# Kernel tuning notes

Hardware: AMD Instinct MI355X
Metric: run time of the kernel (lower is better)

Reference implementation:

```python
import jax, jax.numpy as jnp
import numpy as np

# FreqDecoupledBlock: Mamba(d_model=dim, d_state=16, d_conv=4, expand=2) spatial branch
# + rFFT2 magnitude filter (1x1 conv -> ReLU -> 1x1 conv) branch, fused, then two 1x1 heads.

D_STATE = 16
D_CONV = 4
EXPAND = 2


def setup_inputs() -> dict:
    key = jax.random.key(0)
    B, C, H, W = 4, 64, 128, 128
    d_model = C
    d_inner = EXPAND * d_model
    dt_rank = (d_model + 15) // 16
    ks = jax.random.split(key, 18)
    g = lambda k, shp, sc: jax.random.normal(k, shp, jnp.float32) * sc
    return {
        "x": g(ks[0], (B, C, H, W), 1.0),
        # Mamba params (in_proj/x_proj/out_proj are bias-free as in mamba_ssm defaults)
        "W_in": g(ks[1], (d_model, 2 * d_inner), d_model ** -0.5),
        "conv_w": g(ks[2], (d_inner, D_CONV), 0.3),
        "conv_b": g(ks[3], (d_inner,), 0.1),
        "W_xproj": g(ks[4], (d_inner, dt_rank + 2 * D_STATE), d_inner ** -0.5),
        "W_dt": g(ks[5], (dt_rank, d_inner), dt_rank ** -0.5),
        "b_dt": g(ks[6], (d_inner,), 0.3) - 4.0,  # softplus -> small positive dt
        "A_log": jnp.tile(jnp.log(jnp.arange(1.0, D_STATE + 1.0, dtype=jnp.float32)), (d_inner, 1)),
        "D": jnp.ones((d_inner,), jnp.float32),
        "W_out": g(ks[7], (d_inner, d_model), d_inner ** -0.5),
        # freq_filter: Conv2d(C,C,1) -> ReLU -> Conv2d(C,C,1)
        "Wf1": g(ks[8], (C, C), C ** -0.5), "bf1": g(ks[9], (C,), 0.05),
        "Wf2": g(ks[10], (C, C), C ** -0.5), "bf2": g(ks[11], (C,), 0.05),
        # output heads
        "W_enh": g(ks[12], (C, C), C ** -0.5), "b_enh": g(ks[13], (C,), 0.05),
        "W_seg": g(ks[14], (C, C), C ** -0.5), "b_seg": g(ks[15], (C,), 0.05),
    }


def _silu(v):
    return v * jax.nn.sigmoid(v)


def _mamba(xf, W_in, conv_w, conv_b, W_xproj, W_dt, b_dt, A_log, D, W_out):
    # xf: (B, L, d_model)
    B, L, _ = xf.shape
    d_inner = W_in.shape[1] // 2
    dt_rank = W_dt.shape[0]
    d_state = A_log.shape[1]
    xz = xf @ W_in                                   # (B,L,2*d_inner)
    x_in, z = jnp.split(xz, 2, axis=-1)
    # depthwise causal conv1d (kernel D_CONV) along L
    xp = jnp.pad(x_in, ((0, 0), (D_CONV - 1, 0), (0, 0)))
    xc = conv_b
    for k in range(D_CONV):
        xc = xc + conv_w[:, k] * xp[:, k:k + L, :]
    xc = _silu(xc)                                   # (B,L,d_inner)
    dbc = xc @ W_xproj
    dt = jax.nn.softplus(dbc[..., :dt_rank] @ W_dt + b_dt)      # (B,L,d_inner)
    Bm = dbc[..., dt_rank:dt_rank + d_state]                    # (B,L,d_state)
    Cm = dbc[..., dt_rank + d_state:]                           # (B,L,d_state)
    A = -jnp.exp(A_log)                                          # (d_inner,d_state)

    def step(h, inps):
        xt, dtt, Bt, Ct = inps                       # (B,d_inner),(B,d_inner),(B,d_state),(B,d_state)
        dA = jnp.exp(dtt[..., None] * A)             # (B,d_inner,d_state)
        h = h * dA + (dtt * xt)[..., None] * Bt[:, None, :]
        y = jnp.einsum('bds,bs->bd', h, Ct)
        return h, y

    h0 = jnp.zeros((B, d_inner, d_state), xf.dtype)
    seq = (xc.transpose(1, 0, 2), dt.transpose(1, 0, 2), Bm.transpose(1, 0, 2), Cm.transpose(1, 0, 2))
    _, ys = jax.lax.scan(step, h0, seq)              # (L,B,d_inner)
    y = ys.transpose(1, 0, 2) + xc * D
    y = y * _silu(z)
    return y @ W_out                                 # (B,L,d_model)


def _conv1x1(v, Wc, bc):
    return jnp.einsum('oc,bchw->bohw', Wc, v) + bc[:, None, None]


def reference(x, W_in, conv_w, conv_b, W_xproj, W_dt, b_dt, A_log, D, W_out,
              Wf1, bf1, Wf2, bf2, W_enh, b_enh, W_seg, b_seg):
    B, C, H, W = x.shape
    # spatial branch: Mamba over flattened H*W tokens
    xf = x.transpose(0, 2, 3, 1).reshape(B, H * W, C)
    x_spatial = _mamba(xf, W_in, conv_w, conv_b, W_xproj, W_dt, b_dt, A_log, D, W_out)
    x_spatial = x_spatial.reshape(B, H, W, C).transpose(0, 3, 1, 2)
    # frequency branch: filter magnitude, keep phase
    Xf = jnp.fft.rfft2(x)                            # (B,C,H,W//2+1) complex
    mag = jnp.abs(Xf)
    pha = jnp.angle(Xf)
    m = jax.nn.relu(_conv1x1(mag, Wf1, bf1))
    m = _conv1x1(m, Wf2, bf2)
    x_freq = jnp.fft.irfft2(m * jnp.exp(1j * pha), s=(H, W))
    fused = x_spatial + x_freq
    feat_enh = _conv1x1(fused, W_enh, b_enh)
    feat_seg = _conv1x1(fused, W_seg, b_seg)
    return (feat_enh, feat_seg)
```

## Files before the change

kernel.cpp:

```cpp
#include <hip/hip_runtime.h>
#include <math.h>

#define BATCH 4
#define CMOD 64
#define HH 128
#define WW 128
#define LSEQ 16384
#define DI 128
#define DSTATE 16
#define DTR 4
#define TCH 64
#define NCHUNK 256

__device__ __forceinline__ float siluf(float v){ return v / (1.f + expf(-v)); }

__global__ void k_prep_w(const float* __restrict__ W_in, const float* __restrict__ W_out,
                         const float* __restrict__ W_xproj,
                         float* __restrict__ WT_in, float* __restrict__ WoT, float* __restrict__ WxT){
  int tid = blockIdx.x*256 + threadIdx.x;
  int stride = gridDim.x*256;
  for (int i=tid; i<256*64; i+=stride){ int o=i>>6, c=i&63; WT_in[i] = W_in[c*256+o]; }
  for (int i=tid; i<64*128; i+=stride){ int o=i>>7, c=i&127; WoT[i] = W_out[c*64+o]; }
  for (int i=tid; i<36*128; i+=stride){ int n=i>>7, c=i&127; WxT[i] = W_xproj[c*36+n]; }
}

__global__ __launch_bounds__(256) void k_in_proj(const float* __restrict__ x,
                                                 const float* __restrict__ WT,
                                                 float* __restrict__ xz){
  __shared__ float sm[256*33];
  int tid  = threadIdx.x;
  int bid  = blockIdx.x;
  int s8   = bid >> 6;
  int xcd  = bid & 7;
  int j    = (bid >> 3) & 7;
  int tile = s8*8 + xcd;
  int q    = j;
  size_t px = (size_t)tile*256 + tid;
  int b = (int)(px >> 14);
  int l = (int)(px & 16383);
  const float* xb = x + (((size_t)b*64)<<14) + l;
  float in[64];
  #pragma unroll
  for (int c=0;c<64;c++) in[c] = xb[((size_t)c)<<14];
  const float* Wq = WT + q*32*64;
  for (int og=0; og<8; ++og){
    const float* w0 = Wq + (og*4+0)*64;
    const float* w1 = Wq + (og*4+1)*64;
    const float* w2 = Wq + (og*4+2)*64;
    const float* w3 = Wq + (og*4+3)*64;
    float a0=0.f,a1=0.f,a2=0.f,a3=0.f;
    #pragma unroll
    for (int c=0;c<64;++c){
      float v = in[c];
      a0 = fmaf(v, w0[c], a0); a1 = fmaf(v, w1[c], a1);
      a2 = fmaf(v, w2[c], a2); a3 = fmaf(v, w3[c], a3);
    }
    float* s = sm + tid*33 + og*4;
    s[0]=a0; s[1]=a1; s[2]=a2; s[3]=a3;
  }
  __syncthreads();
  size_t rowbase = (size_t)tile*256*256 + (size_t)q*32;
  #pragma unroll
  for (int i=0;i<8;i++){
    int idx = i*256 + tid;
    int r   = idx >> 3;
    int c4  = idx & 7;
    const float* s = sm + r*33 + c4*4;
    ((float4*)(xz + rowbase + (size_t)r*256))[c4] = make_float4(s[0],s[1],s[2],s[3]);
  }
}

__global__ void k_conv_silu(const float* __restrict__ xz, const float* __restrict__ conv_w,
                            const float* __restrict__ conv_b, float* __restrict__ xc){
  size_t gid = (size_t)blockIdx.x*256 + threadIdx.x;
  int d = (int)(gid & 127);
  int l = (int)((gid >> 7) & (LSEQ-1));
  int b = (int)(gid >> 21);
  const float* base = xz + (((size_t)b)<<14)*256;
  float acc = conv_b[d];
  #pragma unroll
  for (int k=0;k<4;k++){
    int li = l + k - 3;
    if (li >= 0) acc = fmaf(conv_w[d*4+k], base[(size_t)li*256 + d], acc);
  }
  xc[gid] = siluf(acc);
}

__global__ __launch_bounds__(256) void k_xproj_dt(const float* __restrict__ xc,
                         const float* __restrict__ WxT, const float* __restrict__ W_dt,
                         const float* __restrict__ b_dt,
                         float* __restrict__ dtb, float* __restrict__ Bm, float* __restrict__ Cm){
  int tile = blockIdx.x & 255;
  int q    = blockIdx.x >> 8;
  int tid  = threadIdx.x;
  size_t px = (size_t)tile*256 + tid;
  const float4* row = (const float4*)(xc + px*128);
  if (q < 2){
    __shared__ float sout[256*17];
    #pragma unroll
    for (int half=0; half<2; ++half){
      float acc[8];
      #pragma unroll
      for (int n=0;n<8;n++) acc[n]=0.f;
      const float* Wbase = WxT + (4 + q*16 + half*8)*128;
      #pragma unroll 4
      for (int c4=0; c4<32; c4++){
        float4 v = row[c4];
        #pragma unroll
        for (int n=0;n<8;n++){
          const float4 w = *(const float4*)(Wbase + n*128 + c4*4);
          acc[n] = fmaf(v.w, w.w, fmaf(v.z, w.z, fmaf(v.y, w.y, fmaf(v.x, w.x, acc[n]))));
        }
      }
      float* s = sout + tid*17 + half*8;
      #pragma unroll
      for (int n=0;n<8;n++) s[n] = acc[n];
    }
    __syncthreads();
    float* dst = (q==0 ? Bm : Cm) + (size_t)tile*256*16;
    #pragma unroll
    for (int i=0;i<16;i++){
      int idx = i*256 + tid;
      int r = idx >> 4, j = idx & 15;
      dst[r*16 + j] = sout[r*17 + j];
    }
  } else {
    float d0=0.f,d1=0.f,d2=0.f,d3=0.f;
    #pragma unroll 4
    for (int c4=0; c4<32; c4++){
      float4 v = row[c4];
      const float4 w0 = *(const float4*)(WxT + 0*128 + c4*4);
      const float4 w1 = *(const float4*)(WxT + 1*128 + c4*4);
      const float4 w2 = *(const float4*)(WxT + 2*128 + c4*4);
      const float4 w3 = *(const float4*)(WxT + 3*128 + c4*4);
      d0 = fmaf(v.w, w0.w, fmaf(v.z, w0.z, fmaf(v.y, w0.y, fmaf(v.x, w0.x, d0))));
      d1 = fmaf(v.w, w1.w, fmaf(v.z, w1.z, fmaf(v.y, w1.y, fmaf(v.x, w1.x, d1))));
      d2 = fmaf(v.w, w2.w, fmaf(v.z, w2.z, fmaf(v.y, w2.y, fmaf(v.x, w2.x, d2))));
      d3 = fmaf(v.w, w3.w, fmaf(v.z, w3.z, fmaf(v.y, w3.y, fmaf(v.x, w3.x, d3))));
    }
    float4* dtout = (float4*)(dtb + px*128);
    for (int dg=0; dg<32; dg++){
      float r[4];
      #pragma unroll
      for (int j=0;j<4;j++){
        int d = dg*4+j;
        float v = b_dt[d];
        v = fmaf(d0, W_dt[0*128+d], v);
        v = fmaf(d1, W_dt[1*128+d], v);
        v = fmaf(d2, W_dt[2*128+d], v);
        v = fmaf(d3, W_dt[3*128+d], v);
        r[j] = (v > 20.f) ? v : log1pf(expf(v));
      }
      dtout[dg] = make_float4(r[0],r[1],r[2],r[3]);
    }
  }
}

__global__ __launch_bounds__(128) void k_scan1(const float* __restrict__ dtb, const float* __restrict__ xc,
                      const float* __restrict__ Bm, const float* __restrict__ A_log,
                      float* __restrict__ S, float* __restrict__ E1){
  int d = threadIdx.x;
  int ck = blockIdx.x & (NCHUNK-1);
  int b  = blockIdx.x >> 8;
  int t0 = ck*TCH;
  float a0 = -expf(A_log[d*16]);
  __shared__ float sB[16][16];
  float h[16];
  #pragma unroll
  for (int s=0;s<16;s++) h[s]=0.f;
  float dtsum = 0.f;
  size_t rowbase = ((size_t)b<<14);
  for (int tt=0; tt<TCH; tt+=16){
    __syncthreads();
    for (int i=threadIdx.x; i<256; i+=128){
      int tr=i>>4, s=i&15;
      sB[tr][s] = Bm[(rowbase + t0+tt+tr)*16 + s];
    }
    __syncthreads();
    for (int q=0;q<16;q++){
      size_t t = rowbase + t0+tt+q;
      float dtv = dtb[t*128 + d];
      float xcv = xc [t*128 + d];
      float e1 = expf(dtv * a0);
      float du = dtv * xcv;
      dtsum += dtv;
      float f = e1;
      #pragma unroll
      for (int s=0;s<16;s++){ h[s] = fmaf(h[s], f, du*sB[q][s]); f *= e1; }
    }
  }
  size_t idx = (((size_t)b*DI + d)<<8) + ck;
  E1[idx] = expf(dtsum*a0);
  float4* Sp = (float4*)(S + idx*16);
  Sp[0]=make_float4(h[0],h[1],h[2],h[3]);   Sp[1]=make_float4(h[4],h[5],h[6],h[7]);
  Sp[2]=make_float4(h[8],h[9],h[10],h[11]); Sp[3]=make_float4(h[12],h[13],h[14],h[15]);
}

__global__ __launch_bounds__(256) void k_scan2(const float* __restrict__ S, const float* __restrict__ E1,
                        float* __restrict__ Hent){
  int bd = blockIdx.x;
  int k  = threadIdx.x;
  size_t base = (size_t)bd*NCHUNK;
  float p = E1[base + k];
  float h[16];
  {
    const float4* Sp = (const float4*)(S + (base+k)*16);
    float4 a0=Sp[0],a1=Sp[1],a2=Sp[2],a3=Sp[3];
    h[0]=a0.x;h[1]=a0.y;h[2]=a0.z;h[3]=a0.w; h[4]=a1.x;h[5]=a1.y;h[6]=a1.z;h[7]=a1.w;
    h[8]=a2.x;h[9]=a2.y;h[10]=a2.z;h[11]=a2.w; h[12]=a3.x;h[13]=a3.y;h[14]=a3.z;h[15]=a3.w;
  }
  __shared__ float sp[256];
  __shared__ float sh[256][17];
  sp[k] = p;
  #pragma unroll
  for (int s=0;s<16;s++) sh[k][s] = h[s];
  for (int off=1; off<NCHUNK; off<<=1){
    __syncthreads();
    float pl = 1.f; float hl[16];
    if (k >= off){
      pl = sp[k-off];
      #pragma unroll
      for (int s=0;s<16;s++) hl[s] = sh[k-off][s];
    }
    __syncthreads();
    if (k >= off){
      float f = p;
      #pragma unroll
      for (int s=0;s<16;s++){ h[s] = fmaf(hl[s], f, h[s]); f *= p; }
      p *= pl;
      sp[k] = p;
      #pragma unroll
      for (int s=0;s<16;s++) sh[k][s] = h[s];
    }
  }
  if (k == 0){
    float4* H0 = (float4*)(Hent + base*16);
    float4 z = make_float4(0.f,0.f,0.f,0.f);
    H0[0]=z; H0[1]=z; H0[2]=z; H0[3]=z;
  }
  if (k < NCHUNK-1){
    float4* Hp = (float4*)(Hent + (base+k+1)*16);
    Hp[0]=make_float4(h[0],h[1],h[2],h[3]);   Hp[1]=make_float4(h[4],h[5],h[6],h[7]);
    Hp[2]=make_float4(h[8],h[9],h[10],h[11]); Hp[3]=make_float4(h[12],h[13],h[14],h[15]);
  }
}

__global__ __launch_bounds__(128) void k_scan3(const float* __restrict__ dtb, const float* __restrict__ xc,
                      const float* __restrict__ Bm, const float* __restrict__ Cm,
                      const float* __restrict__ A_log, const float* __restrict__ Dw,
                      const float* __restrict__ xz, const float* __restrict__ Hent,
                      float* __restrict__ ym){
  int d = threadIdx.x;
  int ck = blockIdx.x & (NCHUNK-1);
  int b  = blockIdx.x >> 8;
  int t0 = ck*TCH;
  float a0 = -expf(A_log[d*16]);
  float Dv = Dw[d];
  __shared__ float sB[16][16], sC[16][16];
  float h[16];
  {
    const float4* hp = (const float4*)(Hent + ((((size_t)b*DI + d)<<8) + ck)*16);
    float4 v0=hp[0], v1=hp[1], v2=hp[2], v3=hp[3];
    h[0]=v0.x;h[1]=v0.y;h[2]=v0.z;h[3]=v0.w; h[4]=v1.x;h[5]=v1.y;h[6]=v1.z;h[7]=v1.w;
    h[8]=v2.x;h[9]=v2.y;h[10]=v2.z;h[11]=v2.w; h[12]=v3.x;h[13]=v3.y;h[14]=v3.z;h[15]=v3.w;
  }
  size_t rowbase = ((size_t)b<<14);
  for (int tt=0; tt<TCH; tt+=16){
    __syncthreads();
    for (int i=threadIdx.x;i<256;i+=128){
      int tr=i>>4, s=i&15;
      sB[tr][s] = Bm[(rowbase+t0+tt+tr)*16+s];
      sC[tr][s] = Cm[(rowbase+t0+tt+tr)*16+s];
    }
    __syncthreads();
    for (int q=0;q<16;q++){
      size_t t = rowbase + t0+tt+q;
      float dtv = dtb[t*128+d];
      float xcv = xc [t*128+d];
      float e1 = expf(dtv*a0);
      float du = dtv*xcv;
      float f = e1, y=0.f;
      #pragma unroll
      for (int s=0;s<16;s++){
        h[s] = fmaf(h[s], f, du*sB[q][s]);
        y = fmaf(h[s], sC[q][s], y);
        f *= e1;
      }
      float zv = xz[t*256 + 128 + d];
      ym[t*128+d] = (y + xcv*Dv) * siluf(zv);
    }
  }
}

__global__ __launch_bounds__(256) void k_out_proj(const float* __restrict__ ym,
                                                  const float* __restrict__ WoT,
                                                  float* __restrict__ xsp){
  int tile = blockIdx.x >> 2;
  int q    = blockIdx.x & 3;
  size_t px = (size_t)tile*256 + threadIdx.x;
  const float4* row = (const float4*)(ym + px*128);
  float acc[16];
  #pragma unroll
  for (int n=0;n<16;n++) acc[n]=0.f;
  const float* Wq = WoT + q*16*128;
  for (int ci=0; ci<4; ci++){
    float in[32];
    #pragma unroll
    for (int i=0;i<8;i++){ float4 v=row[ci*8+i]; in[4*i]=v.x; in[4*i+1]=v.y; in[4*i+2]=v.z; in[4*i+3]=v.w; }
    #pragma unroll
    for (int n=0;n<16;n++){
      const float* w = Wq + n*128 + ci*32;
      float a = acc[n];
      #pragma unroll
      for (int c=0;c<32;c++) a = fmaf(in[c], w[c], a);
      acc[n] = a;
    }
  }
  float4* out = (float4*)(xsp + px*64) + q*4;
  out[0]=make_float4(acc[0],acc[1],acc[2],acc[3]);
  out[1]=make_float4(acc[4],acc[5],acc[6],acc[7]);
  out[2]=make_float4(acc[8],acc[9],acc[10],acc[11]);
  out[3]=make_float4(acc[12],acc[13],acc[14],acc[15]);
}

__device__ __forceinline__ int br7(int x){ return (int)(__brev((unsigned)x) >> 25); }

__device__ __forceinline__ void fft128(float2* s, int lane, float sign){
  #pragma unroll
  for (int stage=0; stage<7; ++stage){
    __syncthreads();
    int half = 1<<stage;
    int pos = lane & (half-1);
    int i0 = ((lane >> stage) << (stage+1)) | pos;
    int i1 = i0 + half;
    float ang = sign * (-6.2831853071795864769f) * (float)pos / (float)(half*2);
    float sn, cs;
    __sincosf(ang, &sn, &cs);
    float2 a = s[i0], b = s[i1];
    float tr = fmaf(b.x, cs, -b.y*sn);
    float ti = fmaf(b.x, sn,  b.y*cs);
    s[i0] = make_float2(a.x+tr, a.y+ti);
    s[i1] = make_float2(a.x-tr, a.y-ti);
  }
  __syncthreads();
}

__global__ __launch_bounds__(256) void k_fft_row(const float* __restrict__ x, float2* __restrict__ Xrow){
  __shared__ float2 sm[4][128];
  int lane = threadIdx.x & 63;
  int f = threadIdx.x >> 6;
  size_t row = (size_t)blockIdx.x*4 + f;
  const float* xr = x + row*128;
  float2* s = sm[f];
  s[br7(lane)]    = make_float2(xr[lane], 0.f);
  s[br7(lane+64)] = make_float2(xr[lane+64], 0.f);
  fft128(s, lane, 1.f);
  float2* o = Xrow + row*65;
  o[lane] = s[lane];
  if (lane==0) o[64] = s[64];
}

__global__ __launch_bounds__(256) void k_fft_col(const float2* __restrict__ Xrow,
                                                 float2* __restrict__ Xf, float* __restrict__ magb){
  __shared__ float2 sm[4][128];
  int lane = threadIdx.x & 63;
  int f = threadIdx.x >> 6;
  int fid = blockIdx.x*4 + f;
  int bin = fid % 65;
  int bc  = fid / 65;
  const float2* src = Xrow + (size_t)bc*8320 + bin;
  float2* s = sm[f];
  s[br7(lane)]    = src[(size_t)lane*65];
  s[br7(lane+64)] = src[(size_t)(lane+64)*65];
  fft128(s, lane, 1.f);
  float2* dst = Xf + (size_t)bc*8320 + bin;
  float*  mg  = magb + (size_t)bc*8320 + bin;
  float2 v0 = s[lane], v1 = s[lane+64];
  dst[(size_t)lane*65] = v0;
  dst[(size_t)(lane+64)*65] = v1;
  mg[(size_t)lane*65] = sqrtf(v0.x*v0.x + v0.y*v0.y);
  mg[(size_t)(lane+64)*65] = sqrtf(v1.x*v1.x + v1.y*v1.y);
}

__global__ __launch_bounds__(256) void k_freq_mlp(const float* __restrict__ magb,
                        const float2* __restrict__ Xf,
                        const float* __restrict__ Wf1, const float* __restrict__ bf1,
                        const float* __restrict__ Wf2, const float* __restrict__ bf2,
                        float2* __restrict__ Yspec){
  __shared__ float sW1[4096];
  __shared__ float sW2[4096];
  __shared__ float smm[4096];
  __shared__ float shh[4096];
  int tid = threadIdx.x;
  int p   = tid & 63;
  int hq  = tid >> 6;
  int b    = blockIdx.x / 130;
  int rem0 = blockIdx.x*64 - b*8320;
  const float* mbase = magb + (size_t)b*532480 + rem0;
  #pragma unroll
  for (int i=0;i<16;i++){
    int idx = i*256 + tid;
    int o = idx >> 6, c = idx & 63;
    sW1[c*64 + o] = Wf1[idx];
    sW2[c*64 + o] = Wf2[idx];
  }
  #pragma unroll
  for (int i=0;i<16;i++){
    int c = i*4 + hq;
    smm[c*64 + p] = mbase[(size_t)c*8320 + p];
  }
  __syncthreads();
  float acc[16];
  #pragma unroll
  for (int j=0;j<16;j++) acc[j] = bf1[hq*16+j];
  #pragma unroll 4
  for (int c=0;c<64;c++){
    float mv = smm[c*64 + p];
    const float4* wr = (const float4*)(sW1 + c*64 + hq*16);
    float4 w0=wr[0], w1=wr[1], w2=wr[2], w3=wr[3];
    acc[0]=fmaf(w0.x,mv,acc[0]); acc[1]=fmaf(w0.y,mv,acc[1]);
    acc[2]=fmaf(w0.z,mv,acc[2]); acc[3]=fmaf(w0.w,mv,acc[3]);
    acc[4]=fmaf(w1.x,mv,acc[4]); acc[5]=fmaf(w1.y,mv,acc[5]);
    acc[6]=fmaf(w1.z,mv,acc[6]); acc[7]=fmaf(w1.w,mv,acc[7]);
    acc[8]=fmaf(w2.x,mv,acc[8]); acc[9]=fmaf(w2.y,mv,acc[9]);
    acc[10]=fmaf(w2.z,mv,acc[10]); acc[11]=fmaf(w2.w,mv,acc[11]);
    acc[12]=fmaf(w3.x,mv,acc[12]); acc[13]=fmaf(w3.y,mv,acc[13]);
    acc[14]=fmaf(w3.z,mv,acc[14]); acc[15]=fmaf(w3.w,mv,acc[15]);
  }
  #pragma unroll
  for (int j=0;j<16;j++) shh[(hq*16+j)*64 + p] = fmaxf(acc[j], 0.f);
  __syncthreads();
  #pragma unroll
  for (int j=0;j<16;j++) acc[j] = bf2[hq*16+j];
  #pragma unroll 4
  for (int c=0;c<64;c++){
    float hv = shh[c*64 + p];
    const float4* wr = (const float4*)(sW2 + c*64 + hq*16);
    float4 w0=wr[0], w1=wr[1], w2=wr[2], w3=wr[3];
    acc[0]=fmaf(w0.x,hv,acc[0]); acc[1]=fmaf(w0.y,hv,acc[1]);
    acc[2]=fmaf(w0.z,hv,acc[2]); acc[3]=fmaf(w0.w,hv,acc[3]);
    acc[4]=fmaf(w1.x,hv,acc[4]); acc[5]=fmaf(w1.y,hv,acc[5]);
    acc[6]=fmaf(w1.z,hv,acc[6]); acc[7]=fmaf(w1.w,hv,acc[7]);
    acc[8]=fmaf(w2.x,hv,acc[8]); acc[9]=fmaf(w2.y,hv,acc[9]);
    acc[10]=fmaf(w2.z,hv,acc[10]); acc[11]=fmaf(w2.w,hv,acc[11]);
    acc[12]=fmaf(w3.x,hv,acc[12]); acc[13]=fmaf(w3.y,hv,acc[13]);
    acc[14]=fmaf(w3.z,hv,acc[14]); acc[15]=fmaf(w3.w,hv,acc[15]);
  }
  const float2* Xbase = Xf + (size_t)b*532480 + rem0;
  float2* Ybase = Yspec + (size_t)b*532480 + rem0;
  #pragma unroll
  for (int j=0;j<16;j++){
    int o = hq*16 + j;
    size_t off = (size_t)o*8320 + p;
    float mg = mbase[off];
    float2 X = Xbase[off];
    float2 Y;
    if (mg > 0.f){ float sc = acc[j]/mg; Y = make_float2(X.x*sc, X.y*sc); }
    else Y = make_float2(acc[j], 0.f);
    Ybase[off] = Y;
  }
}

__global__ __launch_bounds__(256) void k_ifft_col(const float2* __restrict__ Yspec,
                                                  float2* __restrict__ Zrow){
  __shared__ float2 sm[4][128];
  int lane = threadIdx.x & 63;
  int f = threadIdx.x >> 6;
  int fid = blockIdx.x*4 + f;
  int bin = fid % 65;
  int bc  = fid / 65;
  const float2* src = Yspec + (size_t)bc*8320 + bin;
  float2* s = sm[f];
  s[br7(lane)]    = src[(size_t)lane*65];
  s[br7(lane+64)] = src[(size_t)(lane+64)*65];
  fft128(s, lane, -1.f);
  const float inv = 1.f/128.f;
  float2* dst = Zrow + (size_t)bc*8320 + bin;
  float2 v0 = s[lane], v1 = s[lane+64];
  dst[(size_t)lane*65]      = make_float2(v0.x*inv, v0.y*inv);
  dst[(size_t)(lane+64)*65] = make_float2(v1.x*inv, v1.y*inv);
}

__global__ __launch_bounds__(256) void k_ifft_row(const float2* __restrict__ Zrow,
                                                  float* __restrict__ xfreq){
  __shared__ float2 sm[4][128];
  int lane = threadIdx.x & 63;
  int f = threadIdx.x >> 6;
  size_t row = (size_t)blockIdx.x*4 + f;
  const float2* zr = Zrow + row*65;
  float2* s = sm[f];
  float2 v0 = zr[lane];
  float2 v1;
  if (lane==0) v1 = zr[64];
  else { float2 t = zr[64-lane]; v1 = make_float2(t.x, -t.y); }
  s[br7(lane)]    = v0;
  s[br7(lane+64)] = v1;
  fft128(s, lane, -1.f);
  const float inv = 1.f/128.f;
  float* o = xfreq + row*128;
  o[lane]    = s[lane].x * inv;
  o[lane+64] = s[lane+64].x * inv;
}

__global__ __launch_bounds__(256) void k_fuse_out(const float* __restrict__ xsp,
                       const float* __restrict__ xfreq,
                       const float* __restrict__ W_enh, const float* __restrict__ b_enh,
                       const float* __restrict__ W_seg, const float* __restrict__ b_seg,
                       float* __restrict__ out){
  int tile = blockIdx.x & 255;
  int q    = blockIdx.x >> 8;
  size_t px = (size_t)tile*256 + threadIdx.x;
  int b = (int)(px >> 14);
  int l = (int)(px & 16383);
  float fu[64];
  const float4* sp = (const float4*)(xsp + px*64);
  #pragma unroll
  for (int i=0;i<16;i++){ float4 v=sp[i]; fu[4*i]=v.x; fu[4*i+1]=v.y; fu[4*i+2]=v.z; fu[4*i+3]=v.w; }
  const float* fbase = xfreq + (((size_t)b*64)<<14) + l;
  #pragma unroll
  for (int c=0;c<64;c++) fu[c] += fbase[((size_t)c)<<14];
  const float* Wm = (q < 2) ? W_enh : W_seg;
  const float* bm = (q < 2) ? b_enh : b_seg;
  float* ob = out + ((q < 2) ? (size_t)0 : (size_t)4194304) + (((size_t)b*64)<<14) + l;
  int o0 = (q & 1) * 32;
  for (int og=0; og<8; og++){
    int ob0 = o0 + og*4;
    float a0 = bm[ob0+0], a1 = bm[ob0+1], a2 = bm[ob0+2], a3 = bm[ob0+3];
    const float* w0 = Wm + (ob0+0)*64;
    const float* w1 = Wm + (ob0+1)*64;
    const float* w2 = Wm + (ob0+2)*64;
    const float* w3 = Wm + (ob0+3)*64;
    #pragma unroll
    for (int c=0;c<64;c++){
      float v = fu[c];
      a0 = fmaf(w0[c], v, a0); a1 = fmaf(w1[c], v, a1);
      a2 = fmaf(w2[c], v, a2); a3 = fmaf(w3[c], v, a3);
    }
    ob[((size_t)(ob0+0))<<14] = a0;
    ob[((size_t)(ob0+1))<<14] = a1;
    ob[((size_t)(ob0+2))<<14] = a2;
    ob[((size_t)(ob0+3))<<14] = a3;
  }
}

extern "C" void kernel_launch(void* const* d_in, const int* in_sizes, int n_in,
                              void* d_out, int out_size, void* d_ws, size_t ws_size,
                              hipStream_t stream) {
  const float* x      = (const float*)d_in[0];
  const float* W_in   = (const float*)d_in[1];
  const float* conv_w = (const float*)d_in[2];
  const float* conv_b = (const float*)d_in[3];
  const float* W_xproj= (const float*)d_in[4];
  const float* W_dt   = (const float*)d_in[5];
  const float* b_dt   = (const float*)d_in[6];
  const float* A_log  = (const float*)d_in[7];
  const float* Dw     = (const float*)d_in[8];
  const float* W_out  = (const float*)d_in[9];
  const float* Wf1    = (const float*)d_in[10];
  const float* bf1    = (const float*)d_in[11];
  const float* Wf2    = (const float*)d_in[12];
  const float* bf2    = (const float*)d_in[13];
  const float* W_enh  = (const float*)d_in[14];
  const float* b_enh  = (const float*)d_in[15];
  const float* W_seg  = (const float*)d_in[16];
  const float* b_seg  = (const float*)d_in[17];
  float* out = (float*)d_out;

  float* W = (float*)d_ws;
  size_t o = 0;
  float* xf   = W + o; o += 4194304;
  float* xz   = W + o; o += 16777216;
  float* xcb  = W + o; o += 8388608;
  float* dtb  = W + o; o += 8388608;
  float* Bm   = W + o; o += 1048576;
  float* Cm   = W + o; o += 1048576;
  float* Sb   = W + o; o += 2097152;
  float* E1   = W + o; o += 131072;
  float* Hent = W + o; o += 2097152;
  float* ymb  = W + o; o += 8388608;
  float* xsp  = W + o; o += 4194304;
  float* WT_in= W + o; o += 16384;
  float* WoT  = W + o; o += 8192;
  float* WxT  = W + o; o += 4608;
  float2* Xrow  = (float2*)dtb;
  float2* Yspec = (float2*)dtb;
  float2* Xfb   = (float2*)xcb;
  float2* Zrow  = (float2*)xcb;
  float*  magb  = Sb;
  float*  xfreq = xf;
  (void)ws_size; (void)in_sizes; (void)n_in; (void)out_size;

  k_prep_w<<<28,256,0,stream>>>(W_in, W_out, W_xproj, WT_in, WoT, WxT);
  k_in_proj<<<2048,256,0,stream>>>(x, WT_in, xz);
  k_conv_silu<<<32768,256,0,stream>>>(xz, conv_w, conv_b, xcb);
  k_xproj_dt<<<768,256,0,stream>>>(xcb, WxT, W_dt, b_dt, dtb, Bm, Cm);
  k_scan1<<<1024,128,0,stream>>>(dtb, xcb, Bm, A_log, Sb, E1);
  k_scan2<<<512,256,0,stream>>>(Sb, E1, Hent);
  k_scan3<<<1024,128,0,stream>>>(dtb, xcb, Bm, Cm, A_log, Dw, xz, Hent, ymb);
  k_out_proj<<<1024,256,0,stream>>>(ymb, WoT, xsp);
  k_fft_row<<<8192,256,0,stream>>>(x, Xrow);
  k_fft_col<<<4160,256,0,stream>>>(Xrow, Xfb, magb);
  k_freq_mlp<<<520,256,0,stream>>>(magb, Xfb, Wf1, bf1, Wf2, bf2, Yspec);
  k_ifft_col<<<4160,256,0,stream>>>(Yspec, Zrow);
  k_ifft_row<<<8192,256,0,stream>>>(Zrow, xfreq);
  k_fuse_out<<<1024,256,0,stream>>>(xsp, xfreq, W_enh, b_enh, W_seg, b_seg, out);
}
```

Before: 576.0 us.

## Fuse causal depthwise conv and SiLU into input projection kernel

The input projection kernel now applies the depthwise causal conv and SiLU directly to the x half of its output in shared memory. It recomputes a 3-row halo from the input so that blocks do not depend on each other. The z half goes to a compact 128-wide buffer, and the separate conv kernel is removed. This avoids writing and re-reading the full interleaved xz tensor. In exchange, each block does some redundant halo computation and the shared-memory indexing gets more complex with rotated bank offsets.

```diff
diff --git a/kernel.cpp b/kernel.cpp
--- a/kernel.cpp
+++ b/kernel.cpp
@@ -26,15 +26,18 @@
 
 __global__ __launch_bounds__(256) void k_in_proj(const float* __restrict__ x,
                                                  const float* __restrict__ WT,
-                                                 float* __restrict__ xz){
-  __shared__ float sm[256*33];
+                                                 const float* __restrict__ conv_w,
+                                                 const float* __restrict__ conv_b,
+                                                 float* __restrict__ zb,
+                                                 float* __restrict__ xcb){
+  __shared__ float sm[8448];
   int tid  = threadIdx.x;
   int bid  = blockIdx.x;
   int s8   = bid >> 6;
   int xcd  = bid & 7;
-  int j    = (bid >> 3) & 7;
+  int jj   = (bid >> 3) & 7;
   int tile = s8*8 + xcd;
-  int q    = j;
+  int q    = jj;
   size_t px = (size_t)tile*256 + tid;
   int b = (int)(px >> 14);
   int l = (int)(px & 16383);
@@ -55,35 +58,65 @@
       a0 = fmaf(v, w0[c], a0); a1 = fmaf(v, w1[c], a1);
       a2 = fmaf(v, w2[c], a2); a3 = fmaf(v, w3[c], a3);
     }
-    float* s = sm + tid*33 + og*4;
-    s[0]=a0; s[1]=a1; s[2]=a2; s[3]=a3;
-  }
-  __syncthreads();
-  size_t rowbase = (size_t)tile*256*256 + (size_t)q*32;
-  #pragma unroll
-  for (int i=0;i<8;i++){
-    int idx = i*256 + tid;
-    int r   = idx >> 3;
-    int c4  = idx & 7;
-    const float* s = sm + r*33 + c4*4;
-    ((float4*)(xz + rowbase + (size_t)r*256))[c4] = make_float4(s[0],s[1],s[2],s[3]);
-  }
-}
-
-__global__ void k_conv_silu(const float* __restrict__ xz, const float* __restrict__ conv_w,
-                            const float* __restrict__ conv_b, float* __restrict__ xc){
-  size_t gid = (size_t)blockIdx.x*256 + threadIdx.x;
-  int d = (int)(gid & 127);
-  int l = (int)((gid >> 7) & (LSEQ-1));
-  int b = (int)(gid >> 21);
-  const float* base = xz + (((size_t)b)<<14)*256;
-  float acc = conv_b[d];
-  #pragma unroll
-  for (int k=0;k<4;k++){
-    int li = l + k - 3;
-    if (li >= 0) acc = fmaf(conv_w[d*4+k], base[(size_t)li*256 + d], acc);
-  }
-  xc[gid] = siluf(acc);
+    int col = og*4;
+    sm[tid*32 + ((col+0+tid)&31)] = a0;
+    sm[tid*32 + ((col+1+tid)&31)] = a1;
+    sm[tid*32 + ((col+2+tid)&31)] = a2;
+    sm[tid*32 + ((col+3+tid)&31)] = a3;
+  }
+  if (q < 4){
+    bool first = ((tile & 63) == 0);
+    if (tid < 96 && !first){
+      int brow = tid >> 5, ch = tid & 31;
+      size_t pxb = (size_t)tile*256 - 3 + brow;
+      int bb = (int)(pxb >> 14);
+      int lb = (int)(pxb & 16383);
+      const float* xrb = x + (((size_t)bb*64)<<14) + lb;
+      const float* w = Wq + ch*64;
+      float a = 0.f;
+      #pragma unroll
+      for (int c=0;c<64;c++) a = fmaf(xrb[((size_t)c)<<14], w[c], a);
+      sm[8192 + brow*32 + ch] = a;
+    }
+    if (tid < 128){
+      int k = tid >> 5, ch = tid & 31;
+      sm[8288 + tid] = conv_w[(q*32 + ch)*4 + k];
+    }
+    if (tid < 32) sm[8416 + tid] = conv_b[q*32 + tid];
+    __syncthreads();
+    float* xcbase = xcb + (size_t)tile*256*128 + (size_t)q*32;
+    for (int p=0;p<32;p++){
+      int idx = p*256 + tid;
+      int r  = idx >> 5;
+      int ch = idx & 31;
+      float acc = sm[8416 + ch];
+      #pragma unroll
+      for (int k=0;k<4;k++){
+        int rr = r + k - 3;
+        bool have = (rr >= 0) || (!first);
+        if (have){
+          float xv = (rr >= 0) ? sm[rr*32 + ((ch+rr)&31)]
+                               : sm[8192 + (rr+3)*32 + ch];
+          acc = fmaf(sm[8288 + k*32 + ch], xv, acc);
+        }
+      }
+      xcbase[(size_t)r*128 + ch] = siluf(acc);
+    }
+  } else {
+    __syncthreads();
+    size_t rowbase = (size_t)tile*256*128 + (size_t)(q-4)*32;
+    #pragma unroll
+    for (int i=0;i<8;i++){
+      int idx = i*256 + tid;
+      int r   = idx >> 3;
+      int c4  = idx & 7;
+      float v0 = sm[r*32 + ((c4*4+0+r)&31)];
+      float v1 = sm[r*32 + ((c4*4+1+r)&31)];
+      float v2 = sm[r*32 + ((c4*4+2+r)&31)];
+      float v3 = sm[r*32 + ((c4*4+3+r)&31)];
+      ((float4*)(zb + rowbase + (size_t)r*128))[c4] = make_float4(v0,v1,v2,v3);
+    }
+  }
 }
 
 __global__ __launch_bounds__(256) void k_xproj_dt(const float* __restrict__ xc,
@@ -248,7 +281,7 @@
 __global__ __launch_bounds__(128) void k_scan3(const float* __restrict__ dtb, const float* __restrict__ xc,
                       const float* __restrict__ Bm, const float* __restrict__ Cm,
                       const float* __restrict__ A_log, const float* __restrict__ Dw,
-                      const float* __restrict__ xz, const float* __restrict__ Hent,
+                      const float* __restrict__ zb, const float* __restrict__ Hent,
                       float* __restrict__ ym){
   int d = threadIdx.x;
   int ck = blockIdx.x & (NCHUNK-1);
@@ -286,7 +319,7 @@
         y = fmaf(h[s], sC[q][s], y);
         f *= e1;
       }
-      float zv = xz[t*256 + 128 + d];
+      float zv = zb[t*128 + d];
       ym[t*128+d] = (y + xcv*Dv) * siluf(zv);
     }
   }
@@ -569,7 +602,7 @@
   float* W = (float*)d_ws;
   size_t o = 0;
   float* xf   = W + o; o += 4194304;
-  float* xz   = W + o; o += 16777216;
+  float* zb   = W + o; o += 16777216;
   float* xcb  = W + o; o += 8388608;
   float* dtb  = W + o; o += 8388608;
   float* Bm   = W + o; o += 1048576;
@@ -591,12 +624,11 @@
   (void)ws_size; (void)in_sizes; (void)n_in; (void)out_size;
 
   k_prep_w<<<28,256,0,stream>>>(W_in, W_out, W_xproj, WT_in, WoT, WxT);
-  k_in_proj<<<2048,256,0,stream>>>(x, WT_in, xz);
-  k_conv_silu<<<32768,256,0,stream>>>(xz, conv_w, conv_b, xcb);
+  k_in_proj<<<2048,256,0,stream>>>(x, WT_in, conv_w, conv_b, zb, xcb);
   k_xproj_dt<<<768,256,0,stream>>>(xcb, WxT, W_dt, b_dt, dtb, Bm, Cm);
   k_scan1<<<1024,128,0,stream>>>(dtb, xcb, Bm, A_log, Sb, E1);
   k_scan2<<<512,256,0,stream>>>(Sb, E1, Hent);
-  k_scan3<<<1024,128,0,stream>>>(dtb, xcb, Bm, Cm, A_log, Dw, xz, Hent, ymb);
+  k_scan3<<<1024,128,0,stream>>>(dtb, xcb, Bm, Cm, A_log, Dw, zb, Hent, ymb);
   k_out_proj<<<1024,256,0,stream>>>(ymb, WoT, xsp);
   k_fft_row<<<8192,256,0,stream>>>(x, Xrow);
   k_fft_col<<<4160,256,0,stream>>>(Xrow, Xfb, magb);
```

Result: faster. 533.5 us (-7.4%).
